# Kernel tuning notes

Measured on AMD Instinct MI355X. Metric: run time of the kernel, lower is better.

## Reference

```python
import jax, jax.numpy as jnp
import numpy as np

EPS = 1e-12  # torch F.normalize eps

def _l2norm(v, axis):
    n = jnp.sqrt(jnp.sum(v * v, axis=axis, keepdims=True))
    return v / jnp.maximum(n, EPS)

def setup_inputs() -> dict:
    key = jax.random.key(0)
    k1, k2, k3 = jax.random.split(key, 3)
    N, C, H, W, K = 64, 512, 32, 32, 64
    x = jax.random.normal(k1, (N, C, H, W), dtype=jnp.float32)
    conv_w = jax.random.normal(k2, (K, C), dtype=jnp.float32) * 0.05
    centroids = jax.random.uniform(k3, (K, C), dtype=jnp.float32)
    return {"x": x, "conv_w": conv_w, "centroids": centroids}

def reference(x, conv_w, centroids):
    N, C, H, W = x.shape
    K = centroids.shape[0]
    # descriptor-wise L2 normalization over channel dim
    x = _l2norm(x, axis=1)
    xf = x.reshape(N, C, H * W)                       # (N, C, S)
    # 1x1 conv (no bias) == per-pixel matmul, then softmax over clusters
    logits = jnp.einsum('kc,ncs->nks', conv_w, xf)    # (N, K, S)
    a = jax.nn.softmax(logits, axis=1)                # softmax over clusters
    # vlad[n,k,:] = sum_s a[n,k,s] * (x[n,:,s] - centroid[k])
    # = (a @ x^T) - centroid * sum_s a   -- two GEMM-like ops, no (N,K,C,S) tensor
    vlad = jnp.einsum('nks,ncs->nkc', a, xf) - a.sum(axis=-1)[..., None] * centroids[None, :, :]
    # intra-normalization per cluster, flatten, global L2 norm
    vlad = _l2norm(vlad, axis=2)
    vlad = vlad.reshape(N, K * C)
    vlad = _l2norm(vlad, axis=1)
    return vlad
```

## Files before the change

kernel.cpp:

```cpp
#include <hip/hip_runtime.h>
#include <hip/hip_bf16.h>
#include <math.h>

#define EPSF 1e-12f

typedef __attribute__((ext_vector_type(8))) short bf16x8;
typedef __attribute__((ext_vector_type(4))) float f32x4;
typedef __attribute__((ext_vector_type(4))) short short4v;
typedef __attribute__((ext_vector_type(4))) unsigned short ushort4v;

static __device__ __forceinline__ short f2bf(float f) {
  union { __hip_bfloat16 h; short s; } u;
  u.h = __float2bfloat16(f);
  return u.s;
}

__global__ __launch_bounds__(256) void k2_mfma(
    const float* __restrict__ x, const float* __restrict__ w,
    unsigned short* __restrict__ ap, float* __restrict__ suma) {
  __shared__ __align__(16) float xf[64][70];
  __shared__ __align__(16) short wb[64][72];
  __shared__ __align__(16) float red[4][64];
  __shared__ float invs[64];
  __shared__ float gmaxs[64];
  __shared__ float gsums[64];

  const int n = blockIdx.y;
  const int s0 = blockIdx.x << 6;
  const int t = threadIdx.x;
  const int lane = t & 63;
  const int wid = t >> 6;
  const int col = t & 15;
  const int quad = (t >> 4) & 3;
  const int cr = t >> 4;
  const int sg = t & 15;

  f32x4 acc[4] = {{0,0,0,0},{0,0,0,0},{0,0,0,0},{0,0,0,0}};
  float ssq0 = 0.f, ssq1 = 0.f, ssq2 = 0.f, ssq3 = 0.f;

  for (int c0 = 0; c0 < 512; c0 += 64) {
#pragma unroll
    for (int p = 0; p < 4; ++p) {
      int c = cr + (p << 4);
      float4 g = *(const float4*)&x[((size_t)((n << 9) + c0 + c) << 10) + s0 + (sg << 2)];
      float2 glo; glo.x = g.x; glo.y = g.y;
      float2 ghi; ghi.x = g.z; ghi.y = g.w;
      *(float2*)&xf[c][sg << 2] = glo;
      *(float2*)&xf[c][(sg << 2) + 2] = ghi;
      ssq0 = fmaf(g.x, g.x, ssq0); ssq1 = fmaf(g.y, g.y, ssq1);
      ssq2 = fmaf(g.z, g.z, ssq2); ssq3 = fmaf(g.w, g.w, ssq3);
      float4 gw = *(const float4*)&w[(c << 9) + c0 + (sg << 2)];
      short4v hw; hw.x = f2bf(gw.x); hw.y = f2bf(gw.y); hw.z = f2bf(gw.z); hw.w = f2bf(gw.w);
      *(short4v*)&wb[c][sg << 2] = hw;
    }
    __syncthreads();
#pragma unroll
    for (int cc = 0; cc < 64; cc += 32) {
      bf16x8 af = *(const bf16x8*)&wb[(wid << 4) + col][cc + (quad << 3)];
      int cb = cc + (quad << 3);
#pragma unroll
      for (int sgr = 0; sgr < 4; ++sgr) {
        int sc = (sgr << 4) + col;
        bf16x8 bfr;
#pragma unroll
        for (int j = 0; j < 8; ++j) bfr[j] = f2bf(xf[cb + j][sc]);
        acc[sgr] = __builtin_amdgcn_mfma_f32_16x16x32_bf16(af, bfr, acc[sgr], 0, 0, 0);
      }
    }
    __syncthreads();
  }

  ssq0 += __shfl_xor(ssq0, 16, 64); ssq0 += __shfl_xor(ssq0, 32, 64);
  ssq1 += __shfl_xor(ssq1, 16, 64); ssq1 += __shfl_xor(ssq1, 32, 64);
  ssq2 += __shfl_xor(ssq2, 16, 64); ssq2 += __shfl_xor(ssq2, 32, 64);
  ssq3 += __shfl_xor(ssq3, 16, 64); ssq3 += __shfl_xor(ssq3, 32, 64);
  if (lane < 16) {
    float4 v; v.x = ssq0; v.y = ssq1; v.z = ssq2; v.w = ssq3;
    *(float4*)&red[wid][sg << 2] = v;
  }
  __syncthreads();
  if (t < 64) {
    float tot = red[0][t] + red[1][t] + red[2][t] + red[3][t];
    invs[t] = 1.0f / fmaxf(sqrtf(tot), EPSF);
  }
  __syncthreads();

  float li[4];
#pragma unroll
  for (int sgr = 0; sgr < 4; ++sgr) li[sgr] = invs[(sgr << 4) + col];
  float le[4][4];
#pragma unroll
  for (int sgr = 0; sgr < 4; ++sgr)
#pragma unroll
    for (int r = 0; r < 4; ++r) le[sgr][r] = acc[sgr][r] * li[sgr];

  float mx[4];
#pragma unroll
  for (int sgr = 0; sgr < 4; ++sgr) {
    float m = fmaxf(fmaxf(le[sgr][0], le[sgr][1]), fmaxf(le[sgr][2], le[sgr][3]));
    m = fmaxf(m, __shfl_xor(m, 16, 64));
    m = fmaxf(m, __shfl_xor(m, 32, 64));
    mx[sgr] = m;
  }
  if (lane < 16) {
#pragma unroll
    for (int sgr = 0; sgr < 4; ++sgr) red[wid][(sgr << 4) + sg] = mx[sgr];
  }
  __syncthreads();
  if (t < 64)
    gmaxs[t] = fmaxf(fmaxf(red[0][t], red[1][t]), fmaxf(red[2][t], red[3][t]));
  __syncthreads();

  float ps[4];
#pragma unroll
  for (int sgr = 0; sgr < 4; ++sgr) {
    float gm = gmaxs[(sgr << 4) + col];
    float p = 0.f;
#pragma unroll
    for (int r = 0; r < 4; ++r) {
      float e = __expf(le[sgr][r] - gm);
      le[sgr][r] = e;
      p += e;
    }
    p += __shfl_xor(p, 16, 64);
    p += __shfl_xor(p, 32, 64);
    ps[sgr] = p;
  }
  if (lane < 16) {
#pragma unroll
    for (int sgr = 0; sgr < 4; ++sgr) red[wid][(sgr << 4) + sg] = ps[sgr];
  }
  __syncthreads();
  if (t < 64) gsums[t] = red[0][t] + red[1][t] + red[2][t] + red[3][t];
  __syncthreads();

  float sk[4] = {0.f, 0.f, 0.f, 0.f};
#pragma unroll
  for (int sgr = 0; sgr < 4; ++sgr) {
    float rinv = 1.0f / gsums[(sgr << 4) + col];
#pragma unroll
    for (int r = 0; r < 4; ++r) {
      float av = le[sgr][r] * rinv;
      sk[r] += av;
      float apv = av * li[sgr];
      int k = (wid << 4) + (quad << 2) + r;
      ap[((size_t)((n << 6) + k) << 10) + s0 + (sgr << 4) + col] =
          (unsigned short)f2bf(apv);
    }
  }
#pragma unroll
  for (int r = 0; r < 4; ++r) {
    sk[r] += __shfl_xor(sk[r], 1, 64);
    sk[r] += __shfl_xor(sk[r], 2, 64);
    sk[r] += __shfl_xor(sk[r], 4, 64);
    sk[r] += __shfl_xor(sk[r], 8, 64);
  }
  if (col == 0) {
#pragma unroll
    for (int r = 0; r < 4; ++r)
      atomicAdd(&suma[(n << 6) + (wid << 4) + (quad << 2) + r], sk[r]);
  }
}

__global__ __launch_bounds__(256) void k3_mfma(
    const float* __restrict__ x, const unsigned short* __restrict__ ap,
    const float* __restrict__ cent, const float* __restrict__ suma,
    float* __restrict__ out, float* __restrict__ rnorm2) {
  __shared__ __align__(16) char sm[64 * 72 * 2 * 2];
  short (*xb)[72] = reinterpret_cast<short(*)[72]>(sm);
  short (*at)[72] = reinterpret_cast<short(*)[72]>(sm + 9216);
  float (*lt)[68] = reinterpret_cast<float(*)[68]>(sm);

  const int n = blockIdx.y;
  const int c0 = blockIdx.x << 6;
  const int t = threadIdx.x;
  const int lane = t & 63;
  const int wid = t >> 6;
  const int col = t & 15;
  const int quad = (t >> 4) & 3;
  const int cr = t >> 4;
  const int sg = t & 15;

  f32x4 acc[4] = {{0,0,0,0},{0,0,0,0},{0,0,0,0},{0,0,0,0}};

  for (int s0 = 0; s0 < 1024; s0 += 64) {
#pragma unroll
    for (int p = 0; p < 4; ++p) {
      int c = cr + (p << 4);
      float4 g = *(const float4*)&x[((size_t)((n << 9) + c0 + c) << 10) + s0 + (sg << 2)];
      short4v hx; hx.x = f2bf(g.x); hx.y = f2bf(g.y); hx.z = f2bf(g.z); hx.w = f2bf(g.w);
      *(short4v*)&xb[c][sg << 2] = hx;
      ushort4v a4 = *(const ushort4v*)&ap[((size_t)((n << 6) + c) << 10) + s0 + (sg << 2)];
      *(ushort4v*)&at[c][sg << 2] = a4;
    }
    __syncthreads();
#pragma unroll
    for (int ss = 0; ss < 64; ss += 32) {
      bf16x8 af = *(const bf16x8*)&xb[(wid << 4) + col][ss + (quad << 3)];
#pragma unroll
      for (int kt = 0; kt < 4; ++kt) {
        bf16x8 bfr = *(const bf16x8*)&at[(kt << 4) + col][ss + (quad << 3)];
        acc[kt] = __builtin_amdgcn_mfma_f32_16x16x32_bf16(af, bfr, acc[kt], 0, 0, 0);
      }
    }
    __syncthreads();
  }

  float sa[4];
#pragma unroll
  for (int kt = 0; kt < 4; ++kt) sa[kt] = suma[(n << 6) + (kt << 4) + col];
  const int crow = (wid << 4) + (quad << 2);
  float r2[4] = {0.f, 0.f, 0.f, 0.f};
#pragma unroll
  for (int kt = 0; kt < 4; ++kt) {
    int k = (kt << 4) + col;
#pragma unroll
    for (int r = 0; r < 4; ++r) {
      int c = crow + r;
      float ce = cent[(k << 9) + c0 + c];
      float val = acc[kt][r] - sa[kt] * ce;
      r2[kt] = fmaf(val, val, r2[kt]);
      lt[k][c] = val;
    }
  }
#pragma unroll
  for (int kt = 0; kt < 4; ++kt) {
    r2[kt] += __shfl_xor(r2[kt], 16, 64);
    r2[kt] += __shfl_xor(r2[kt], 32, 64);
  }
  if (lane < 16) {
#pragma unroll
    for (int kt = 0; kt < 4; ++kt)
      atomicAdd(&rnorm2[(n << 6) + (kt << 4) + sg], r2[kt]);
  }
  __syncthreads();
#pragma unroll
  for (int u = 0; u < 4; ++u) {
    int k = t >> 2;
    int c = ((t & 3) << 2) + (u << 4);
    float4 v = *(const float4*)&lt[k][c];
    *(float4*)&out[((size_t)((n << 6) + k) << 9) + c0 + c] = v;
  }
}

__global__ __launch_bounds__(64) void k4_factors(const float* __restrict__ rnorm2,
                                                 float* __restrict__ fac) {
  int n = blockIdx.x, k = threadIdx.x;
  float r2 = rnorm2[(n << 6) + k];
  float rn = sqrtf(r2);
  float f = 1.0f / fmaxf(rn, EPSF);
  float nr = rn * f;
  float g = nr * nr;
#pragma unroll
  for (int off = 32; off > 0; off >>= 1) g += __shfl_xor(g, off, 64);
  fac[(n << 6) + k] = f * (1.0f / fmaxf(sqrtf(g), EPSF));
}

__global__ __launch_bounds__(256) void k5_scale(const float* __restrict__ vlad,
                                                const float* __restrict__ fac,
                                                float* __restrict__ out) {
  int idx = blockIdx.x * 256 + threadIdx.x;
  float4 v = ((const float4*)vlad)[idx];
  float f = fac[idx >> 7];
  float4 o;
  o.x = v.x * f; o.y = v.y * f; o.z = v.z * f; o.w = v.w * f;
  ((float4*)out)[idx] = o;
}

extern "C" void kernel_launch(void* const* d_in, const int* in_sizes, int n_in,
                              void* d_out, int out_size, void* d_ws, size_t ws_size,
                              hipStream_t stream) {
  (void)in_sizes; (void)n_in; (void)out_size; (void)ws_size;
  const float* x = (const float*)d_in[0];
  const float* w = (const float*)d_in[1];
  const float* cent = (const float*)d_in[2];
  float* out = (float*)d_out;

  float* ws = (float*)d_ws;
  float* suma = ws;
  float* rnorm2 = ws + 4096;
  float* fac = ws + 8192;
  unsigned short* ap = (unsigned short*)(ws + 12288);

  hipMemsetAsync(ws, 0, 8192 * sizeof(float), stream);
  k2_mfma<<<dim3(16, 64), 256, 0, stream>>>(x, w, ap, suma);
  k3_mfma<<<dim3(8, 64), 256, 0, stream>>>(x, ap, cent, suma, out, rnorm2);
  k4_factors<<<64, 64, 0, stream>>>(rnorm2, fac);
  k5_scale<<<2048, 256, 0, stream>>>(out, fac, out);
}
```

Baseline: 256.5 us.

## Preload bf16 weight fragments in registers and transpose x tile in LDS

The whole conv weight fragment for each wave is converted to bf16 once and kept in 16 registers, so the per-iteration weight global loads and LDS staging go away. The x tile is converted to bf16 at load time and then transposed in shared memory, so the MFMA B operand becomes one vector LDS read instead of eight scalar reads with per-element conversion. This adds an extra barrier and transpose pass per channel chunk and raises register pressure from the fully unrolled loop and the preloaded fragments.

Result: slower. 289.9 us (+13.0%).

```diff
diff --git a/kernel.cpp b/kernel.cpp
--- a/kernel.cpp
+++ b/kernel.cpp
@@ -18,8 +18,8 @@
 __global__ __launch_bounds__(256) void k2_mfma(
     const float* __restrict__ x, const float* __restrict__ w,
     unsigned short* __restrict__ ap, float* __restrict__ suma) {
-  __shared__ __align__(16) float xf[64][70];
-  __shared__ __align__(16) short wb[64][72];
+  __shared__ __align__(16) short xb[64][72];
+  __shared__ __align__(16) short xt[64][72];
   __shared__ __align__(16) float red[4][64];
   __shared__ float invs[64];
   __shared__ float gmaxs[64];
@@ -35,35 +35,47 @@
   const int cr = t >> 4;
   const int sg = t & 15;
 
+  bf16x8 wf[16];
+#pragma unroll
+  for (int f = 0; f < 16; ++f) {
+    const float* wp = &w[(size_t)(((wid << 4) + col) << 9) + (f << 5) + (quad << 3)];
+    float4 l0 = *(const float4*)wp;
+    float4 l1 = *(const float4*)(wp + 4);
+    wf[f][0] = f2bf(l0.x); wf[f][1] = f2bf(l0.y);
+    wf[f][2] = f2bf(l0.z); wf[f][3] = f2bf(l0.w);
+    wf[f][4] = f2bf(l1.x); wf[f][5] = f2bf(l1.y);
+    wf[f][6] = f2bf(l1.z); wf[f][7] = f2bf(l1.w);
+  }
+
   f32x4 acc[4] = {{0,0,0,0},{0,0,0,0},{0,0,0,0},{0,0,0,0}};
   float ssq0 = 0.f, ssq1 = 0.f, ssq2 = 0.f, ssq3 = 0.f;
 
+#pragma unroll
   for (int c0 = 0; c0 < 512; c0 += 64) {
 #pragma unroll
     for (int p = 0; p < 4; ++p) {
       int c = cr + (p << 4);
       float4 g = *(const float4*)&x[((size_t)((n << 9) + c0 + c) << 10) + s0 + (sg << 2)];
-      float2 glo; glo.x = g.x; glo.y = g.y;
-      float2 ghi; ghi.x = g.z; ghi.y = g.w;
-      *(float2*)&xf[c][sg << 2] = glo;
-      *(float2*)&xf[c][(sg << 2) + 2] = ghi;
       ssq0 = fmaf(g.x, g.x, ssq0); ssq1 = fmaf(g.y, g.y, ssq1);
       ssq2 = fmaf(g.z, g.z, ssq2); ssq3 = fmaf(g.w, g.w, ssq3);
-      float4 gw = *(const float4*)&w[(c << 9) + c0 + (sg << 2)];
-      short4v hw; hw.x = f2bf(gw.x); hw.y = f2bf(gw.y); hw.z = f2bf(gw.z); hw.w = f2bf(gw.w);
-      *(short4v*)&wb[c][sg << 2] = hw;
+      short4v h; h.x = f2bf(g.x); h.y = f2bf(g.y); h.z = f2bf(g.z); h.w = f2bf(g.w);
+      *(short4v*)&xb[c][sg << 2] = h;
+    }
+    __syncthreads();
+#pragma unroll
+    for (int i = 0; i < 2; ++i) {
+      int g = (wid << 1) + i;
+      bf16x8 v = *(const bf16x8*)&xb[lane][g << 3];
+#pragma unroll
+      for (int j = 0; j < 8; ++j) xt[(g << 3) + j][lane] = v[j];
     }
     __syncthreads();
 #pragma unroll
     for (int cc = 0; cc < 64; cc += 32) {
-      bf16x8 af = *(const bf16x8*)&wb[(wid << 4) + col][cc + (quad << 3)];
-      int cb = cc + (quad << 3);
+      bf16x8 af = wf[(c0 >> 5) + (cc >> 5)];
 #pragma unroll
       for (int sgr = 0; sgr < 4; ++sgr) {
-        int sc = (sgr << 4) + col;
-        bf16x8 bfr;
-#pragma unroll
-        for (int j = 0; j < 8; ++j) bfr[j] = f2bf(xf[cb + j][sc]);
+        bf16x8 bfr = *(const bf16x8*)&xt[(sgr << 4) + col][cc + (quad << 3)];
         acc[sgr] = __builtin_amdgcn_mfma_f32_16x16x32_bf16(af, bfr, acc[sgr], 0, 0, 0);
       }
     }
```
